# Performance work log

Measured on AMD Instinct MI355X. Metric: run time of the kernel, lower is better.

## Reference

```python
import jax, jax.numpy as jnp
import numpy as np

B, C, DIM = 8, 2048, 512
H = 512  # hidden_dim
NEG_SLOPE = 0.01  # torch LeakyReLU default


def setup_inputs() -> dict:
    key = jax.random.key(0)
    ks = jax.random.split(key, 8)
    features = jax.random.normal(ks[0], (B, C, DIM), dtype=jnp.float32)
    mask = jax.random.uniform(ks[1], (B, C, C), dtype=jnp.float32)
    s = 0.02
    W_w = jax.random.normal(ks[2], (DIM, 3 * H), dtype=jnp.float32) * s
    b_w = jax.random.normal(ks[3], (3 * H,), dtype=jnp.float32) * s
    a_score = jax.random.normal(ks[4], (2 * H,), dtype=jnp.float32) * s
    b_score = jax.random.normal(ks[5], (1,), dtype=jnp.float32) * s
    W_out = jax.random.normal(ks[6], (H, DIM), dtype=jnp.float32) * s
    b_out = jax.random.normal(ks[7], (DIM,), dtype=jnp.float32) * s
    return {"features": features, "mask": mask, "W_w": W_w, "b_w": b_w,
            "a_score": a_score, "b_score": b_score, "W_out": W_out, "b_out": b_out}


def reference(features, mask, W_w, b_w, a_score, b_score, W_out, b_out):
    # qkv projection: [B,C,3H]
    qkv = features @ W_w + b_w
    q, k, v = jnp.split(qkv, 3, axis=-1)  # each [B,C,H]
    # score(cat([q_i, k_j])) = q_i . a[:H] + k_j . a[H:] + b  (Linear(2H,1))
    sq = q @ a_score[:H]            # [B,C]
    sk = k @ a_score[H:]            # [B,C]
    scores = jax.nn.leaky_relu(sq[:, :, None] + sk[:, None, :] + b_score[0],
                               negative_slope=NEG_SLOPE)  # [B,C,C]
    attn = jax.nn.softmax(scores * mask, axis=-1)           # [B,C,C]
    weighted = jnp.einsum('bij,bjh->bih', attn, v)          # [B,C,H]
    return weighted @ W_out + b_out                          # [B,C,DIM]
```

## Files before the change

### kernel.cpp

```cpp
#include <hip/hip_runtime.h>
#include <hip/hip_bf16.h>

#define B_ 8
#define C_ 2048
#define DIM_ 512
#define NEG_SLOPE 0.01f

typedef short bf16x8 __attribute__((ext_vector_type(8)));
typedef short bf16x4 __attribute__((ext_vector_type(4)));
typedef float f32x4 __attribute__((ext_vector_type(4)));

#define WT_OFF   0
#define UT_OFF   524288
#define FP_OFF   (524288 + 16777216)
#define BCOMB_F  0
#define WQ_F     512
#define WK_F     1024
#define CQB_F    1536
#define CK_F     1537
#define SQP_F    2048
#define SKP_F    18432

static __device__ __forceinline__ unsigned short bf16u(float x) {
    union { __hip_bfloat16 h; unsigned short u; } c;
    c.h = __float2bfloat16(x);
    return c.u;
}

__global__ __launch_bounds__(256) void k_prep(const float* __restrict__ W_w,
                                              const float* __restrict__ W_out,
                                              const float* __restrict__ b_w,
                                              const float* __restrict__ a_score,
                                              const float* __restrict__ b_score,
                                              char* wsb, float* wsf) {
    __shared__ float As[32][34];
    __shared__ float Bs[32][34];
    __shared__ float s1[256], s2[256];
    const int t = threadIdx.x;
    const int bid = blockIdx.x;

    if (bid == 0) {
        s1[t] = b_w[t] * a_score[t] + b_w[t + 256] * a_score[t + 256];
        s2[t] = b_w[512 + t] * a_score[512 + t] + b_w[768 + t] * a_score[768 + t];
        __syncthreads();
        for (int off = 128; off > 0; off >>= 1) {
            if (t < off) { s1[t] += s1[t + off]; s2[t] += s2[t + off]; }
            __syncthreads();
        }
        if (t == 0) { wsf[CQB_F] = s1[0] + b_score[0]; wsf[CK_F] = s2[0]; }
        __syncthreads();
    }

    if (bid >= 128) {
        int wave = t >> 6, lane = t & 63;
        int e = (bid - 128) * 4 + wave;
        const float4* R4 = (const float4*)(W_w + (size_t)e * 1536);
        const float4* A4 = (const float4*)a_score;
        float aq = 0.f, ak = 0.f;
#pragma unroll
        for (int k = 0; k < 2; ++k) {
            float4 f = R4[lane + 64 * k];
            float4 a = A4[lane + 64 * k];
            aq += f.x * a.x + f.y * a.y + f.z * a.z + f.w * a.w;
            float4 g = R4[128 + lane + 64 * k];
            float4 a2 = A4[128 + lane + 64 * k];
            ak += g.x * a2.x + g.y * a2.y + g.z * a2.z + g.w * a2.w;
        }
#pragma unroll
        for (int off = 32; off; off >>= 1) { aq += __shfl_xor(aq, off); ak += __shfl_xor(ak, off); }
        if (lane == 0) { wsf[WQ_F + e] = aq; wsf[WK_F + e] = ak; }
    }

    const int d0 = (bid & 15) * 32;
    const int e0 = (bid >> 4) * 32;
    const int ty = t >> 4, tx = t & 15;
    const int hl = t >> 5, c = t & 31;
    float a00 = 0.f, a01 = 0.f, a10 = 0.f, a11 = 0.f;
    float bc = 0.f;
    for (int k0 = 0; k0 < 512; k0 += 32) {
#pragma unroll
        for (int r = 0; r < 4; ++r) {
            int h = hl + 8 * r;
            As[h][c] = W_out[(size_t)(k0 + h) * 512 + d0 + c];
            Bs[c][h] = W_w[(size_t)(e0 + h) * 1536 + 1024 + k0 + c];
        }
        __syncthreads();
        if (e0 == 0 && t < 32) {
#pragma unroll
            for (int kk = 0; kk < 32; ++kk)
                bc = fmaf(b_w[1024 + k0 + kk], As[kk][t], bc);
        }
#pragma unroll
        for (int kk = 0; kk < 32; ++kk) {
            float2 a2 = *(const float2*)&As[kk][ty * 2];
            float2 b2 = *(const float2*)&Bs[kk][tx * 2];
            a00 = fmaf(a2.x, b2.x, a00);
            a01 = fmaf(a2.x, b2.y, a01);
            a10 = fmaf(a2.y, b2.x, a10);
            a11 = fmaf(a2.y, b2.y, a11);
        }
        __syncthreads();
    }
    unsigned short* Wt = (unsigned short*)(wsb + WT_OFF);
    const int d = d0 + ty * 2, e = e0 + tx * 2;
    Wt[(size_t)d * 512 + e]           = bf16u(a00);
    Wt[(size_t)d * 512 + e + 1]       = bf16u(a01);
    Wt[(size_t)(d + 1) * 512 + e]     = bf16u(a10);
    Wt[(size_t)(d + 1) * 512 + e + 1] = bf16u(a11);
    if (e0 == 0 && t < 32) wsf[BCOMB_F + d0 + t] = bc;
}

__global__ __launch_bounds__(256) void k_ut(const float* __restrict__ F,
                                            char* __restrict__ wsb, float* __restrict__ wsf) {
    __shared__ unsigned short Fb[32][520];
    const int t = threadIdx.x;
    const int bid = blockIdx.x;
    const int b = bid & 7, j0 = (bid >> 3) * 32;
    const unsigned short* Wt = (const unsigned short*)(wsb + WT_OFF);
    unsigned short* Ut = (unsigned short*)(wsb + UT_OFF) + (size_t)b * 512 * 2048;
    const float* Ft = F + ((size_t)(b * C_ + j0)) * 512;

    {
        const int r = t >> 3, g = t & 7;
        const float4* Fr = (const float4*)(F + ((size_t)(b * C_ + j0 + r)) * 512);
        const float4* WQ4 = (const float4*)(wsf + WQ_F);
        const float4* WK4 = (const float4*)(wsf + WK_F);
        float aq = 0.f, ak = 0.f;
#pragma unroll
        for (int cc = 0; cc < 16; ++cc) {
            float4 f = Fr[cc * 8 + g];
            float4 q = WQ4[cc * 8 + g];
            float4 kk = WK4[cc * 8 + g];
            aq += f.x * q.x + f.y * q.y + f.z * q.z + f.w * q.w;
            ak += f.x * kk.x + f.y * kk.y + f.z * kk.z + f.w * kk.w;
        }
        aq += __shfl_xor(aq, 1); aq += __shfl_xor(aq, 2); aq += __shfl_xor(aq, 4);
        ak += __shfl_xor(ak, 1); ak += __shfl_xor(ak, 2); ak += __shfl_xor(ak, 4);
        if (g == 0) {
            wsf[SQP_F + b * C_ + j0 + r] = aq + wsf[CQB_F];
            wsf[SKP_F + b * C_ + j0 + r] = ak + wsf[CK_F];
        }
    }

#pragma unroll
    for (int q = 0; q < 16; ++q) {
        float4 v = *(const float4*)(Ft + (size_t)q * 1024 + t * 4);
        int jr = 2 * q + (t >> 7);
        int e = (t & 127) * 4;
        unsigned int lo = (unsigned int)bf16u(v.x) | ((unsigned int)bf16u(v.y) << 16);
        unsigned int hi = (unsigned int)bf16u(v.z) | ((unsigned int)bf16u(v.w) << 16);
        *(uint2*)&Fb[jr][e] = make_uint2(lo, hi);
    }
    __syncthreads();
    const int l = t & 63, lr = l & 15, lg = l >> 4;
    const int d0 = (t >> 6) * 128;
    f32x4 acc[8][2];
#pragma unroll
    for (int m = 0; m < 8; ++m)
#pragma unroll
        for (int n = 0; n < 2; ++n) acc[m][n] = (f32x4){0.f, 0.f, 0.f, 0.f};
#pragma unroll
    for (int ks = 0; ks < 16; ++ks) {
        bf16x8 af[8], bv[2];
#pragma unroll
        for (int m = 0; m < 8; ++m)
            af[m] = *(const bf16x8*)(Wt + (size_t)(d0 + 16 * m + lr) * 512 + ks * 32 + 8 * lg);
#pragma unroll
        for (int n = 0; n < 2; ++n)
            bv[n] = *(const bf16x8*)&Fb[16 * n + lr][ks * 32 + 8 * lg];
#pragma unroll
        for (int m = 0; m < 8; ++m)
#pragma unroll
            for (int n = 0; n < 2; ++n)
                acc[m][n] = __builtin_amdgcn_mfma_f32_16x16x32_bf16(af[m], bv[n], acc[m][n], 0, 0, 0);
    }
#pragma unroll
    for (int m = 0; m < 8; ++m)
#pragma unroll
        for (int n = 0; n < 2; ++n)
#pragma unroll
            for (int r = 0; r < 4; ++r) {
                int d = d0 + 16 * m + lg * 4 + r;
                int j = j0 + 16 * n + lr;
                Ut[(size_t)d * 2048 + j] = bf16u(acc[m][n][r]);
            }
}

#define BAR asm volatile("s_waitcnt lgkmcnt(0)\n\ts_barrier" ::: "memory");
#define SCHEDB __builtin_amdgcn_sched_barrier(0);

#define MISSUE(M, KT) { \
    M = __builtin_nontemporal_load((const f32x4*)(mrow + (size_t)(KT) * 64)); }

#define PCX(KV, MV, I) { \
    float z = sqv + (KV); z = fmaxf(z, z * NEG_SLOPE) * (MV); \
    z = __expf(z); psum += z; vv[I] = (short)bf16u(z); }

#define PCOMP(M, KT) { \
    const int kt = (KT); \
    float4 ka = *(const float4*)&sk_lds[kt * 64 + pjc * 4]; \
    bf16x4 vv; \
    PCX(ka.x, M[0], 0) PCX(ka.y, M[1], 1) PCX(ka.z, M[2], 2) PCX(ka.w, M[3], 3) \
    *(bf16x4*)(Pbyte + (kt & 1) * 8192 + prow * 128 \
               + (((pjc >> 1) ^ (prow & 7)) << 4) + ((pjc & 1) << 3)) = vv; }

#define LDUT(U, KT) { \
    const int kt = (KT); \
    _Pragma("unroll") \
    for (int n = 0; n < 2; ++n) { \
        const unsigned short* up = Utw + (size_t)(16 * n + lr) * 2048 + kt * 64 + 8 * lg; \
        U[2 * n]     = *(const bf16x8*)up; \
        U[2 * n + 1] = *(const bf16x8*)(up + 32); \
    } }

#define MFMAP(U, KP) { \
    const char* pb = Pbyte + ((KP) & 1) * 8192; \
    _Pragma("unroll") \
    for (int g = 0; g < 4; ++g) { \
        const char* rp = pb + (16 * g + lr) * 128; \
        bf16x8 a0 = *(const bf16x8*)(rp + ((lg ^ (lr & 7)) << 4)); \
        bf16x8 a1 = *(const bf16x8*)(rp + (((4 + lg) ^ (lr & 7)) << 4)); \
        _Pragma("unroll") \
        for (int n = 0; n < 2; ++n) { \
            acc[g][n] = __builtin_amdgcn_mfma_f32_16x16x32_bf16(a0, U[2 * n],     acc[g][n], 0, 0, 0); \
            acc[g][n] = __builtin_amdgcn_mfma_f32_16x16x32_bf16(a1, U[2 * n + 1], acc[g][n], 0, 0, 0); \
        } \
    } }

#define PHASE(UC, UN, MC, MI, KP) { \
    const int kp = (KP); \
    if (kp + 1 < 32) { PCOMP(MC, kp + 1) LDUT(UN, kp + 1) } \
    SCHEDB \
    if (kp + 3 < 32) MISSUE(MI, kp + 3) \
    SCHEDB \
    MFMAP(UC, kp) \
    BAR }

__global__ __launch_bounds__(1024, 1) void k_attn(const float* __restrict__ mask,
                                                  const float* __restrict__ b_out,
                                                  char* __restrict__ wsb,
                                                  float* __restrict__ out) {
    __shared__ unsigned short Pt[2][64][64];
    __shared__ float sk_lds[2048];
    __shared__ float bcbo[512];
    __shared__ float psums[64][16];
    __shared__ float rinvs[64];
    const int t = threadIdx.x;
    const int bid = blockIdx.x;
    const int b = bid & 7, i0 = (bid >> 3) * 64;
    const int w = t >> 6, l = t & 63, lr = l & 15, lg = l >> 4;
    const int prow = t >> 4, pjc = t & 15;
    const float* wsf = (const float*)(wsb + FP_OFF);
    const unsigned short* Utw = (const unsigned short*)(wsb + UT_OFF)
                                + (size_t)b * 512 * 2048 + (size_t)(w * 32) * 2048;
    char* Pbyte = (char*)Pt;
    const float sqv = wsf[SQP_F + b * C_ + i0 + prow];
    const float* mrow = mask + ((size_t)(b * C_ + i0 + prow)) * C_ + pjc * 4;

    if (t < 512) {
        const float* skp = wsf + SKP_F + b * C_;
        *(float4*)&sk_lds[t * 4] = *(const float4*)(skp + t * 4);
        bcbo[t & 511] = wsf[BCOMB_F + (t & 511)] + b_out[t & 511];
    }
    __syncthreads();

    f32x4 m0, m1, m2;
    bf16x8 u0[4], u1[4];
    MISSUE(m0, 0) MISSUE(m1, 1) MISSUE(m2, 2)
    LDUT(u0, 0)

    float psum = 0.f;
    f32x4 acc[4][2];
#pragma unroll
    for (int g = 0; g < 4; ++g)
#pragma unroll
        for (int n = 0; n < 2; ++n) acc[g][n] = (f32x4){0.f, 0.f, 0.f, 0.f};

    PCOMP(m0, 0)
    BAR

    for (int o = 0; o < 5; ++o) {
        const int tb = o * 6;
        PHASE(u0, u1, m1, m0, tb + 0)
        PHASE(u1, u0, m2, m1, tb + 1)
        PHASE(u0, u1, m0, m2, tb + 2)
        PHASE(u1, u0, m1, m0, tb + 3)
        PHASE(u0, u1, m2, m1, tb + 4)
        PHASE(u1, u0, m0, m2, tb + 5)
    }
    PHASE(u0, u1, m1, m0, 30)
    PHASE(u1, u0, m2, m1, 31)

    psums[prow][pjc] = psum;
    __syncthreads();
    if (t < 64) {
        float s = 0.f;
#pragma unroll
        for (int q = 0; q < 4; ++q) {
            float4 p4 = *(const float4*)&psums[t][q * 4];
            s += p4.x + p4.y + p4.z + p4.w;
        }
        rinvs[t] = 1.0f / s;
    }
    __syncthreads();
#pragma unroll
    for (int g = 0; g < 4; ++g) {
#pragma unroll
        for (int r = 0; r < 4; ++r) {
            const int irow = 16 * g + lg * 4 + r;
            const float rv = rinvs[irow];
            float* orow = out + ((size_t)(b * C_ + i0 + irow)) * DIM_ + w * 32;
#pragma unroll
            for (int n = 0; n < 2; ++n)
                orow[16 * n + lr] = acc[g][n][r] * rv + bcbo[w * 32 + 16 * n + lr];
        }
    }
}

extern "C" void kernel_launch(void* const* d_in, const int* in_sizes, int n_in,
                              void* d_out, int out_size, void* d_ws, size_t ws_size,
                              hipStream_t stream) {
    const float* features = (const float*)d_in[0];
    const float* mask     = (const float*)d_in[1];
    const float* W_w      = (const float*)d_in[2];
    const float* b_w      = (const float*)d_in[3];
    const float* a_score  = (const float*)d_in[4];
    const float* b_score  = (const float*)d_in[5];
    const float* W_out    = (const float*)d_in[6];
    const float* b_out    = (const float*)d_in[7];
    float* out = (float*)d_out;
    char* wsb  = (char*)d_ws;
    float* wsf = (float*)(wsb + FP_OFF);

    k_prep<<<256, 256, 0, stream>>>(W_w, W_out, b_w, a_score, b_score, wsb, wsf);
    k_ut<<<512, 256, 0, stream>>>(features, wsb, wsf);
    k_attn<<<256, 1024, 0, stream>>>(mask, b_out, wsb, out);
}
```

Baseline: 136.8 us.

## Double K-tile width to 128 and restructure mask/Ut software pipeline

Each pipeline phase now covers 128 key columns instead of 64. That halves the number of barrier-separated phases (16 instead of 32) and doubles the P tile in LDS. The pipeline changes from three rotating mask registers and two Ut buffers to two mask register pairs and a single Ut buffer. Ut is now loaded at the start of each phase rather than one phase ahead, and the sched_barriers were removed. Fewer barriers and wider bf16x8 LDS writes are intended to cut synchronisation overhead, at the risk of exposing Ut global-load latency and raising register pressure.

Result: slower. 152.9 us (+11.7%).

```diff
diff --git a/kernel.cpp b/kernel.cpp
--- a/kernel.cpp
+++ b/kernel.cpp
@@ -186,11 +186,15 @@
             }
 }
 
-#define BAR asm volatile("s_waitcnt lgkmcnt(0)\n\ts_barrier" ::: "memory");
-#define SCHEDB __builtin_amdgcn_sched_barrier(0);
+
+#define BAR \
+    asm volatile("s_waitcnt lgkmcnt(0)"); \
+    __builtin_amdgcn_s_barrier();
 
 #define MISSUE(M, KT) { \
-    M = __builtin_nontemporal_load((const f32x4*)(mrow + (size_t)(KT) * 64)); }
+    const float* mp = mrow + (size_t)(KT) * 128; \
+    M##a = __builtin_nontemporal_load((const f32x4*)mp); \
+    M##b = __builtin_nontemporal_load((const f32x4*)(mp + 4)); }
 
 #define PCX(KV, MV, I) { \
     float z = sqv + (KV); z = fmaxf(z, z * NEG_SLOPE) * (MV); \
@@ -198,49 +202,48 @@
 
 #define PCOMP(M, KT) { \
     const int kt = (KT); \
-    float4 ka = *(const float4*)&sk_lds[kt * 64 + pjc * 4]; \
-    bf16x4 vv; \
-    PCX(ka.x, M[0], 0) PCX(ka.y, M[1], 1) PCX(ka.z, M[2], 2) PCX(ka.w, M[3], 3) \
-    *(bf16x4*)(Pbyte + (kt & 1) * 8192 + prow * 128 \
-               + (((pjc >> 1) ^ (prow & 7)) << 4) + ((pjc & 1) << 3)) = vv; }
+    float4 ka = *(const float4*)&sk_lds[kt * 128 + pjc * 8]; \
+    float4 kb = *(const float4*)&sk_lds[kt * 128 + pjc * 8 + 4]; \
+    bf16x8 vv; \
+    PCX(ka.x, M##a[0], 0) PCX(ka.y, M##a[1], 1) PCX(ka.z, M##a[2], 2) PCX(ka.w, M##a[3], 3) \
+    PCX(kb.x, M##b[0], 4) PCX(kb.y, M##b[1], 5) PCX(kb.z, M##b[2], 6) PCX(kb.w, M##b[3], 7) \
+    *(bf16x8*)(Pbyte + (kt & 1) * 16384 + prow * 256 + ((pjc ^ (prow & 7)) << 4)) = vv; }
 
 #define LDUT(U, KT) { \
     const int kt = (KT); \
     _Pragma("unroll") \
-    for (int n = 0; n < 2; ++n) { \
-        const unsigned short* up = Utw + (size_t)(16 * n + lr) * 2048 + kt * 64 + 8 * lg; \
-        U[2 * n]     = *(const bf16x8*)up; \
-        U[2 * n + 1] = *(const bf16x8*)(up + 32); \
-    } }
+    for (int n = 0; n < 2; ++n) \
+        _Pragma("unroll") \
+        for (int ks = 0; ks < 4; ++ks) \
+            U[n * 4 + ks] = *(const bf16x8*)(Utw + (size_t)(16 * n + lr) * 2048 \
+                                             + kt * 128 + ks * 32 + 8 * lg); }
 
 #define MFMAP(U, KP) { \
-    const char* pb = Pbyte + ((KP) & 1) * 8192; \
+    const char* pb = Pbyte + ((KP) & 1) * 16384; \
     _Pragma("unroll") \
     for (int g = 0; g < 4; ++g) { \
-        const char* rp = pb + (16 * g + lr) * 128; \
-        bf16x8 a0 = *(const bf16x8*)(rp + ((lg ^ (lr & 7)) << 4)); \
-        bf16x8 a1 = *(const bf16x8*)(rp + (((4 + lg) ^ (lr & 7)) << 4)); \
+        const char* rp = pb + (16 * g + lr) * 256; \
         _Pragma("unroll") \
-        for (int n = 0; n < 2; ++n) { \
-            acc[g][n] = __builtin_amdgcn_mfma_f32_16x16x32_bf16(a0, U[2 * n],     acc[g][n], 0, 0, 0); \
-            acc[g][n] = __builtin_amdgcn_mfma_f32_16x16x32_bf16(a1, U[2 * n + 1], acc[g][n], 0, 0, 0); \
+        for (int ks = 0; ks < 4; ++ks) { \
+            bf16x8 a = *(const bf16x8*)(rp + (((ks * 4 + lg) ^ (lr & 7)) << 4)); \
+            acc[g][0] = __builtin_amdgcn_mfma_f32_16x16x32_bf16(a, U[ks],     acc[g][0], 0, 0, 0); \
+            acc[g][1] = __builtin_amdgcn_mfma_f32_16x16x32_bf16(a, U[4 + ks], acc[g][1], 0, 0, 0); \
         } \
     } }
 
-#define PHASE(UC, UN, MC, MI, KP) { \
+#define PHASE(M, KP) { \
     const int kp = (KP); \
-    if (kp + 1 < 32) { PCOMP(MC, kp + 1) LDUT(UN, kp + 1) } \
-    SCHEDB \
-    if (kp + 3 < 32) MISSUE(MI, kp + 3) \
-    SCHEDB \
-    MFMAP(UC, kp) \
+    LDUT(u, kp) \
+    if (kp + 1 < 16) PCOMP(M, kp + 1) \
+    if (kp + 3 < 16) MISSUE(M, kp + 3) \
+    MFMAP(u, kp) \
     BAR }
 
 __global__ __launch_bounds__(1024, 1) void k_attn(const float* __restrict__ mask,
                                                   const float* __restrict__ b_out,
                                                   char* __restrict__ wsb,
                                                   float* __restrict__ out) {
-    __shared__ unsigned short Pt[2][64][64];
+    __shared__ unsigned short Pt[2][64][128];
     __shared__ float sk_lds[2048];
     __shared__ float bcbo[512];
     __shared__ float psums[64][16];
@@ -255,7 +258,7 @@
                                 + (size_t)b * 512 * 2048 + (size_t)(w * 32) * 2048;
     char* Pbyte = (char*)Pt;
     const float sqv = wsf[SQP_F + b * C_ + i0 + prow];
-    const float* mrow = mask + ((size_t)(b * C_ + i0 + prow)) * C_ + pjc * 4;
+    const float* mrow = mask + ((size_t)(b * C_ + i0 + prow)) * C_ + pjc * 8;
 
     if (t < 512) {
         const float* skp = wsf + SKP_F + b * C_;
@@ -264,11 +267,8 @@
     }
     __syncthreads();
 
-    f32x4 m0, m1, m2;
-    bf16x8 u0[4], u1[4];
-    MISSUE(m0, 0) MISSUE(m1, 1) MISSUE(m2, 2)
-    LDUT(u0, 0)
-
+    f32x4 m0a, m0b, m1a, m1b;
+    bf16x8 u[8];
     float psum = 0.f;
     f32x4 acc[4][2];
 #pragma unroll
@@ -276,20 +276,15 @@
 #pragma unroll
         for (int n = 0; n < 2; ++n) acc[g][n] = (f32x4){0.f, 0.f, 0.f, 0.f};
 
+    MISSUE(m0, 0) MISSUE(m1, 1)
     PCOMP(m0, 0)
+    MISSUE(m0, 2)
     BAR
 
-    for (int o = 0; o < 5; ++o) {
-        const int tb = o * 6;
-        PHASE(u0, u1, m1, m0, tb + 0)
-        PHASE(u1, u0, m2, m1, tb + 1)
-        PHASE(u0, u1, m0, m2, tb + 2)
-        PHASE(u1, u0, m1, m0, tb + 3)
-        PHASE(u0, u1, m2, m1, tb + 4)
-        PHASE(u1, u0, m0, m2, tb + 5)
-    }
-    PHASE(u0, u1, m1, m0, 30)
-    PHASE(u1, u0, m2, m1, 31)
+    for (int o = 0; o < 8; ++o) {
+        PHASE(m1, 2 * o)
+        PHASE(m0, 2 * o + 1)
+    }
 
     psums[prow][pjc] = psum;
     __syncthreads();
```
